# Performance work log

Measured on AMD Instinct MI355X. Metric: run time of the kernel, lower is better.

Reference implementation:

```python
import jax, jax.numpy as jnp
import numpy as np
from jax import lax

NUM_ANCHORS = 3
NUM_CLASSES = 80
SCORE_THRESH = 0.3
NMS_THRESH = 0.45
TOPK = 128  # max kept candidates per class per image (fixed-shape NMS)
REDUCTIONS = (8, 16, 32)
_ANCHORS = np.array([[12, 16], [19, 36], [40, 28], [36, 75], [76, 55], [72, 146],
                     [142, 110], [192, 243], [459, 401]], dtype=np.float32).reshape(3, 3, 2)


def _decode(pred, anchors):
    # pred: [b, A*(5+C), h, w]; anchors: [A,2] already divided by reduction
    b, c, h, w = pred.shape
    p = pred.reshape(b, NUM_ANCHORS, 5 + NUM_CLASSES, h * w).transpose(0, 1, 3, 2)  # [b,A,hw,5+C]
    gx = (jnp.arange(h * w) % w).astype(p.dtype)   # grid x offset per flattened cell
    gy = (jnp.arange(h * w) // w).astype(p.dtype)  # grid y offset
    cx = (jax.nn.sigmoid(p[..., 0]) + gx) / w
    cy = (jax.nn.sigmoid(p[..., 1]) + gy) / h
    bw = jnp.exp(p[..., 2]) * (anchors[:, 0] / w)[None, :, None]
    bh = jnp.exp(p[..., 3]) * (anchors[:, 1] / h)[None, :, None]
    x1 = cx - 0.5 * bw
    y1 = cy - 0.5 * bh
    boxes = jnp.stack([x1, y1, x1 + bw, y1 + bh], axis=-1)  # [b,A,hw,4] xyxy, normalized
    scores = jax.nn.sigmoid(p[..., 4])[..., None] * jax.nn.sigmoid(p[..., 5:])  # [b,A,hw,C]
    return boxes, scores


def _nms_single(boxes, probs):
    # boxes: [N,4]; probs: [N] with below-threshold entries masked to -1.
    # Greedy NMS on top-K candidates sorted by score (same math as the numpy loop).
    vals, idx = lax.top_k(probs, TOPK)
    bx = boxes[idx]                                            # [K,4] sorted by score desc
    area = (bx[:, 2] - bx[:, 0]) * (bx[:, 3] - bx[:, 1])
    tl = jnp.maximum(bx[:, None, :2], bx[None, :, :2])
    br = jnp.minimum(bx[:, None, 2:], bx[None, :, 2:])
    whi = jnp.clip(br - tl, 0.0)
    inter = whi[..., 0] * whi[..., 1]
    iou = inter / (area[:, None] + area[None, :] - inter)      # [K,K]
    ar = jnp.arange(TOPK)

    def step(p, i):
        sup = (iou[i] > NMS_THRESH) & (ar > i) & (p[i] > 0)
        return jnp.where(sup, -1.0, p), None

    p, _ = lax.scan(step, vals, ar)
    keep = p > 0
    return jnp.where(keep[:, None], bx, 0.0), jnp.where(keep, p, 0.0)


def reference(preds0, preds1, preds2):
    boxes_list, score_list = [], []
    for pred, red, anc in zip((preds0, preds1, preds2), REDUCTIONS, _ANCHORS):
        bx, sc = _decode(pred, jnp.asarray(anc) / red)
        boxes_list.append(bx)
        score_list.append(sc)
    boxes = jnp.concatenate(boxes_list, axis=2)
    scores = jnp.concatenate(score_list, axis=2)
    b = boxes.shape[0]
    boxes = boxes.reshape(b, -1, 4)              # [b, N, 4],  N = A * sum(hw)
    scores = scores.reshape(b, -1, NUM_CLASSES)  # [b, N, C]
    probs = jnp.where(scores > SCORE_THRESH, scores, -1.0)
    per_class = jax.vmap(_nms_single, in_axes=(None, 1))        # map over classes
    out_boxes, out_scores = jax.vmap(per_class)(boxes, probs)   # [b,C,K,4], [b,C,K]
    cls_id = jnp.broadcast_to(
        jnp.arange(NUM_CLASSES, dtype=out_boxes.dtype)[None, :, None], out_scores.shape)
    # [b, C, K, 6] = (x1, y1, x2, y2, score, class_id); zeroed rows = no detection
    return jnp.concatenate([out_boxes, out_scores[..., None], cls_id[..., None]], axis=-1)


def setup_inputs():
    key = jax.random.key(0)
    k0, k1, k2 = jax.random.split(key, 3)
    C = NUM_ANCHORS * (5 + NUM_CLASSES)
    return {
        "preds0": jax.random.normal(k0, (16, C, 76, 76), jnp.float32),
        "preds1": jax.random.normal(k1, (16, C, 38, 38), jnp.float32),
        "preds2": jax.random.normal(k2, (16, C, 19, 19), jnp.float32),
    }
```

## Files before the change

kernel.cpp:

```cpp
#include <hip/hip_runtime.h>
#include <math.h>
#include <stdint.h>

#define BATCH 16
#define NCLS 80
#define SUMHW 7581
#define NN 22743
#define ASTRIDE 7584
#define PADNN (3 * ASTRIDE)
#define TOPK 128
#define CAP 1024
#define WCAP 320
#define GMAX (4 * WCAP)
#define PRUNECAP 512
#define KEYBASE 0x3E800000u
#define KB2     0x3F180000u
#define SBITS   0x3F19999Au

typedef float f32x4 __attribute__((ext_vector_type(4)));

__device__ __forceinline__ float sigf(float x) {
    float e = (float)exp(-(double)x);
    return 1.0f / (1.0f + e);
}
__device__ __forceinline__ float expf_cr(float x) {
    return (float)exp((double)x);
}

struct DecParams { float aw[9]; float ah[9]; };

__global__ __launch_bounds__(256) void decode_kernel(
        const float* __restrict__ p0, const float* __restrict__ p1,
        const float* __restrict__ p2,
        float* __restrict__ so_arr, float* __restrict__ xthr_arr) {
    int blk = blockIdx.x;
    int b = blk / 27;
    int rem = blk % 27;
    int a = rem / 9;
    int seg = rem % 9;
    int s, segi;
    if (seg < 6)      { s = 0; segi = seg; }
    else if (seg < 8) { s = 1; segi = seg - 6; }
    else              { s = 2; segi = 0; }
    const int HW_[3]  = {5776, 1444, 361};
    const int OFF_[3] = {0, 5776, 7220};
    const float* __restrict__ pr = (s == 0) ? p0 : (s == 1) ? p1 : p2;
    int HW = HW_[s], OFF = OFF_[s];
    int t = threadIdx.x;

    auto mkthr = [](float so) {
        float thr = __int_as_float(0x7F800000);
        if (so > 0.59999f) {
            double arg = (double)so / 0.59999 - 1.0;
            thr = __double2float_rd(-log(arg));
        }
        return thr;
    };

    if (s != 2) {
        int cell0 = segi * 1024 + t * 4;
        if (cell0 >= HW) return;
        const float4* ob4 =
            (const float4*)(pr + ((size_t)b * 255 + (size_t)a * 85 + 4) * (size_t)HW);
        float4 ov = ob4[cell0 >> 2];
        float4 sov, thv;
        sov.x = sigf(ov.x); thv.x = mkthr(sov.x);
        sov.y = sigf(ov.y); thv.y = mkthr(sov.y);
        sov.z = sigf(ov.z); thv.z = mkthr(sov.z);
        sov.w = sigf(ov.w); thv.w = mkthr(sov.w);
        size_t pidx = (size_t)b * PADNN + a * ASTRIDE + OFF + cell0;
        *(float4*)(so_arr + pidx)   = sov;
        *(float4*)(xthr_arr + pidx) = thv;
    } else {
        const float* ob = pr + ((size_t)b * 255 + (size_t)a * 85 + 4) * 361;
        for (int i = t; i < 361; i += 256) {
            float so = sigf(ob[i]);
            size_t pidx = (size_t)b * PADNN + a * ASTRIDE + 7220 + i;
            so_arr[pidx] = so;
            xthr_arr[pidx] = mkthr(so);
        }
    }
}

__global__ __launch_bounds__(256) void select_nms_kernel(
        const float* __restrict__ p0, const float* __restrict__ p1,
        const float* __restrict__ p2,
        const float* __restrict__ so_arr,
        const float* __restrict__ xthr_arr,
        DecParams dp,
        float* __restrict__ out) {
    __shared__ __attribute__((aligned(16))) unsigned long long wn64[4 * WCAP];
    unsigned long long* skeyF = wn64;
    __shared__ unsigned int kbuf[GMAX];
    __shared__ unsigned long long skeyM[PRUNECAP];
    __shared__ unsigned long long sorted[TOPK];
    __shared__ unsigned long long mskp[2 * TOPK];
    __shared__ float4 bxs4[TOPK];
    __shared__ float pvs[TOPK];
    __shared__ unsigned int hist[512];
    __shared__ unsigned int sums[256];
    __shared__ unsigned int wvc[4];
    __shared__ unsigned long long aliveLDS[2];
    __shared__ unsigned int sh_bin, sh_above, gcount;

    int t = threadIdx.x;
    int w = t >> 6, lane = t & 63;
    int bid = blockIdx.x;
    int b = bid / NCLS;
    int c = bid % NCLS;

    if (t < 4) wvc[t] = 0;
    for (int i = t; i < 512; i += 256) hist[i] = 0;
    __syncthreads();

    auto cmpPushB = [&](f32x4 A0, f32x4 A1, f32x4 A2,
                        f32x4 Q0, f32x4 Q1, f32x4 Q2, int cellb) {
        unsigned m = 0;
        m |= (A0.x > Q0.x) ? 0x001u : 0u;  m |= (A0.y > Q0.y) ? 0x002u : 0u;
        m |= (A0.z > Q0.z) ? 0x004u : 0u;  m |= (A0.w > Q0.w) ? 0x008u : 0u;
        m |= (A1.x > Q1.x) ? 0x010u : 0u;  m |= (A1.y > Q1.y) ? 0x020u : 0u;
        m |= (A1.z > Q1.z) ? 0x040u : 0u;  m |= (A1.w > Q1.w) ? 0x080u : 0u;
        m |= (A2.x > Q2.x) ? 0x100u : 0u;  m |= (A2.y > Q2.y) ? 0x200u : 0u;
        m |= (A2.z > Q2.z) ? 0x400u : 0u;  m |= (A2.w > Q2.w) ? 0x800u : 0u;
        if (m) {
            unsigned pos = atomicAdd(&wvc[w], (unsigned)__popc(m));
            unsigned long long* wl = wn64 + w * WCAP;
#define PKW(bit, val, nn) \
            if (m & (bit)) { if (pos < WCAP) wl[pos] = \
                (((unsigned long long)__float_as_uint(val)) << 32) | (unsigned)(nn); \
                pos++; }
            PKW(0x001u, A0.x, cellb + 0)
            PKW(0x002u, A0.y, cellb + 1)
            PKW(0x004u, A0.z, cellb + 2)
            PKW(0x008u, A0.w, cellb + 3)
            PKW(0x010u, A1.x, SUMHW + cellb + 0)
            PKW(0x020u, A1.y, SUMHW + cellb + 1)
            PKW(0x040u, A1.z, SUMHW + cellb + 2)
            PKW(0x080u, A1.w, SUMHW + cellb + 3)
            PKW(0x100u, A2.x, 2 * SUMHW + cellb + 0)
            PKW(0x200u, A2.y, 2 * SUMHW + cellb + 1)
            PKW(0x400u, A2.z, 2 * SUMHW + cellb + 2)
            PKW(0x800u, A2.w, 2 * SUMHW + cellb + 3)
#undef PKW
        }
    };

    auto scanBlock = [&](const float* __restrict__ pr, int HW, int OFF) {
        const int nq = HW >> 2;
        unsigned long long bx0 = (unsigned long long)(uintptr_t)
            (pr + ((size_t)b * 255 + 0 * 85 + 5 + (size_t)c) * (size_t)HW);
        unsigned long long bx1 = (unsigned long long)(uintptr_t)
            (pr + ((size_t)b * 255 + 1 * 85 + 5 + (size_t)c) * (size_t)HW);
        unsigned long long bx2 = (unsigned long long)(uintptr_t)
            (pr + ((size_t)b * 255 + 2 * 85 + 5 + (size_t)c) * (size_t)HW);
        unsigned long long bq0 = (unsigned long long)(uintptr_t)
            (xthr_arr + (size_t)b * PADNN + 0 * ASTRIDE + OFF);
        unsigned long long bq1 = (unsigned long long)(uintptr_t)
            (xthr_arr + (size_t)b * PADNN + 1 * ASTRIDE + OFF);
        unsigned long long bq2 = (unsigned long long)(uintptr_t)
            (xthr_arr + (size_t)b * PADNN + 2 * ASTRIDE + OFF);
        int i = t;
        for (; i + 256 < nq; i += 512) {
            unsigned vo1 = (unsigned)i << 4;
            unsigned vo2 = (unsigned)(i + 256) << 4;
            f32x4 x0, x1, x2, x3, x4, x5, q0, q1, q2, q3, q4, q5;
            asm volatile(
                "global_load_dwordx4 %0, %12, %14\n\t"
                "global_load_dwordx4 %1, %12, %15\n\t"
                "global_load_dwordx4 %2, %12, %16\n\t"
                "global_load_dwordx4 %3, %13, %14\n\t"
                "global_load_dwordx4 %4, %13, %15\n\t"
                "global_load_dwordx4 %5, %13, %16\n\t"
                "global_load_dwordx4 %6, %12, %17\n\t"
                "global_load_dwordx4 %7, %12, %18\n\t"
                "global_load_dwordx4 %8, %12, %19\n\t"
                "global_load_dwordx4 %9, %13, %17\n\t"
                "global_load_dwordx4 %10, %13, %18\n\t"
                "global_load_dwordx4 %11, %13, %19\n\t"
                "s_waitcnt vmcnt(0)"
                : "=&v"(x0), "=&v"(x1), "=&v"(x2), "=&v"(x3), "=&v"(x4), "=&v"(x5),
                  "=&v"(q0), "=&v"(q1), "=&v"(q2), "=&v"(q3), "=&v"(q4), "=&v"(q5)
                : "v"(vo1), "v"(vo2), "s"(bx0), "s"(bx1), "s"(bx2),
                  "s"(bq0), "s"(bq1), "s"(bq2));
            cmpPushB(x0, x1, x2, q0, q1, q2, OFF + 4 * i);
            cmpPushB(x3, x4, x5, q3, q4, q5, OFF + 4 * (i + 256));
        }
        if (i < nq) {
            unsigned voff = (unsigned)i << 4;
            f32x4 x0, x1, x2, q0, q1, q2;
            asm volatile(
                "global_load_dwordx4 %0, %6, %7\n\t"
                "global_load_dwordx4 %1, %6, %8\n\t"
                "global_load_dwordx4 %2, %6, %9\n\t"
                "global_load_dwordx4 %3, %6, %10\n\t"
                "global_load_dwordx4 %4, %6, %11\n\t"
                "global_load_dwordx4 %5, %6, %12\n\t"
                "s_waitcnt vmcnt(0)"
                : "=&v"(x0), "=&v"(x1), "=&v"(x2),
                  "=&v"(q0), "=&v"(q1), "=&v"(q2)
                : "v"(voff), "s"(bx0), "s"(bx1), "s"(bx2),
                  "s"(bq0), "s"(bq1), "s"(bq2));
            cmpPushB(x0, x1, x2, q0, q1, q2, OFF + 4 * i);
        }
    };
    scanBlock(p0, 5776, 0);
    scanBlock(p1, 1444, 5776);
#pragma unroll
    for (int a = 0; a < 3; ++a) {
        const float* __restrict__ cp =
            p2 + ((size_t)b * 255 + (size_t)a * 85 + 5 + (size_t)c) * 361;
        const float* __restrict__ xt = xthr_arr + (size_t)b * PADNN + a * ASTRIDE + 7220;
        int n0 = a * SUMHW + 7220;
        for (int i = t; i < 361; i += 256) {
            float xv = cp[i];
            if (xv > xt[i]) {
                unsigned pos = atomicAdd(&wvc[w], 1u);
                if (pos < WCAP) wn64[w * WCAP + pos] =
                    (((unsigned long long)__float_as_uint(xv)) << 32) | (unsigned)(n0 + i);
            }
        }
    }
    __syncthreads();

    unsigned cw0 = wvc[0], cw1 = wvc[1], cw2 = wvc[2], cw3 = wvc[3];
    bool ovf = (cw0 > WCAP) || (cw1 > WCAP) || (cw2 > WCAP) || (cw3 > WCAP);
    unsigned G = cw0 + cw1 + cw2 + cw3;
    bool fb = ovf || (G < TOPK);

    auto rankSelect = [&](const unsigned long long* sk, unsigned Gc) {
        if (t < TOPK) sorted[t] = 0ULL;
        __syncthreads();
        unsigned i0 = t, i1 = t + 256, i2 = t + 512, i3 = t + 768;
        bool v0 = i0 < Gc, v1 = i1 < Gc, v2 = i2 < Gc, v3 = i3 < Gc;
        unsigned long long o0 = v0 ? sk[i0] : 0ULL;
        unsigned long long o1 = v1 ? sk[i1] : 0ULL;
        unsigned long long o2 = v2 ? sk[i2] : 0ULL;
        unsigned long long o3 = v3 ? sk[i3] : 0ULL;
        unsigned r0 = 0, r1 = 0, r2 = 0, r3 = 0;
        for (unsigned j = 0; j < Gc; ++j) {
            unsigned long long kj = sk[j];
            r0 += (kj > o0); r1 += (kj > o1); r2 += (kj > o2); r3 += (kj > o3);
        }
        if (v0 && r0 < TOPK) sorted[r0] = o0;
        if (v1 && r1 < TOPK) sorted[r1] = o1;
        if (v2 && r2 < TOPK) sorted[r2] = o2;
        if (v3 && r3 < TOPK) sorted[r3] = o3;
        __syncthreads();
    };

    if (!fb) {
        unsigned woff = 0;
        if (w > 0) woff += cw0;
        if (w > 1) woff += cw1;
        if (w > 2) woff += cw2;
        unsigned mycnt = (w == 0) ? cw0 : (w == 1) ? cw1 : (w == 2) ? cw2 : cw3;
        for (unsigned i = lane; i < mycnt; i += 64) {
            unsigned long long e = wn64[w * WCAP + i];
            float x = __uint_as_float((unsigned)(e >> 32));
            unsigned n = (unsigned)(e & 0xFFFFFFFFu);
            unsigned a = n / SUMHW;
            unsigned r = n - a * SUMHW;
            float so = so_arr[(size_t)b * PADNN + a * ASTRIDE + r];
            float st = 1.0f / (1.0f + __expf(-x));
            unsigned key = __float_as_uint(st * so);
            kbuf[woff + i] = key;
            unsigned bin = (key - KB2) >> 14;
            if (bin > 511u) bin = 511u;
            atomicAdd(&hist[bin], 1u);
        }
        if (t == 0) gcount = 0;
        __syncthreads();

        unsigned m0 = hist[2 * t], m1 = hist[2 * t + 1];
        sums[t] = m0 + m1;
        __syncthreads();
        for (int d = 1; d < 256; d <<= 1) {
            unsigned v = sums[t];
            if (t + d < 256) v += sums[t + d];
            __syncthreads();
            sums[t] = v;
            __syncthreads();
        }
        unsigned si = sums[t], se = si - (m0 + m1);
        if (se < TOPK && TOPK <= si) {
            if (TOPK <= se + m1) { sh_bin = 2 * t + 1; sh_above = se; }
            else                 { sh_bin = 2 * t;     sh_above = se + m1; }
        }
        __syncthreads();
        unsigned B1 = sh_bin, above1 = sh_above;
        unsigned cntB = hist[B1];
        unsigned binlo = KB2 + (B1 << 14);
        if (above1 + cntB > PRUNECAP - 64) {
            fb = true;
        } else {
            unsigned gth = binlo - 256;
            unsigned b1e = cw0, b2e = cw0 + cw1, b3e = b2e + cw2;
            for (unsigned i = t; i < G; i += 256) {
                if (kbuf[i] >= gth) {
                    unsigned pos = atomicAdd(&gcount, 1u);
                    if (pos < PRUNECAP) {
                        unsigned w2, off2;
                        if (i < b1e)      { w2 = 0; off2 = i; }
                        else if (i < b2e) { w2 = 1; off2 = i - b1e; }
                        else if (i < b3e) { w2 = 2; off2 = i - b2e; }
                        else              { w2 = 3; off2 = i - b3e; }
                        unsigned long long e = wn64[w2 * WCAP + off2];
                        float x = __uint_as_float((unsigned)(e >> 32));
                        unsigned n = (unsigned)(e & 0xFFFFFFFFu);
                        unsigned a = n / SUMHW;
                        unsigned r = n - a * SUMHW;
                        float so = so_arr[(size_t)b * PADNN + a * ASTRIDE + r];
                        float ex = so * sigf(x);
                        skeyM[pos] = (ex > 0.3f)
                            ? (((unsigned long long)__float_as_uint(ex) << 32) |
                               (unsigned)(~n))
                            : (unsigned long long)(unsigned)(~n);
                    }
                }
            }
            __syncthreads();
            if (gcount > PRUNECAP) fb = true;
            if (!fb) {
                unsigned Gc = gcount;
                rankSelect(skeyM, Gc);
                bool ok = (Gc >= TOPK) && ((unsigned)(sorted[TOPK - 1] >> 32) >= SBITS);
                if (!ok) fb = true;
            }
        }
    }

    if (fb) {
        auto scanScalar = [&](auto&& body) {
#pragma unroll
            for (int s = 0; s < 3; ++s) {
                const float* __restrict__ pr = (s == 0) ? p0 : (s == 1) ? p1 : p2;
                const int HW  = (s == 0) ? 5776 : (s == 1) ? 1444 : 361;
                const int OFF = (s == 0) ? 0 : (s == 1) ? 5776 : 7220;
#pragma unroll
                for (int a = 0; a < 3; ++a) {
                    const float* __restrict__ cp =
                        pr + ((size_t)b * 255 + (size_t)a * 85 + 5 + (size_t)c) * (size_t)HW;
                    const float* __restrict__ sop =
                        so_arr + (size_t)b * PADNN + a * ASTRIDE + OFF;
                    int n0 = a * SUMHW + OFF;
                    for (int i = t; i < HW; i += 256) {
                        float so = sop[i];
                        if (so <= 0.2999f) continue;
                        float x = cp[i];
                        float st = 1.0f / (1.0f + __expf(-x));
                        float sca = st * so;
                        if (sca > 0.2999f) body(sca, x, so, n0 + i);
                    }
                }
            }
        };
        __syncthreads();
        for (int i = t; i < 512; i += 256) hist[i] = 0;
        if (t == 0) gcount = 0;
        __syncthreads();
        scanScalar([&](float sca, float, float, int) {
            unsigned bin = (__float_as_uint(sca) - KEYBASE) >> 15;
            if (bin > 511u) bin = 511u;
            atomicAdd(&hist[bin], 1u);
        });
        __syncthreads();
        unsigned m0 = hist[2 * t], m1 = hist[2 * t + 1];
        sums[t] = m0 + m1;
        __syncthreads();
        for (int d = 1; d < 256; d <<= 1) {
            unsigned v = sums[t];
            if (t + d < 256) v += sums[t + d];
            __syncthreads();
            sums[t] = v;
            __syncthreads();
        }
        unsigned total = sums[0];
        bool gatherAll = (total < TOPK);
        unsigned gth = 0;
        if (!gatherAll) {
            unsigned si = sums[t], se = si - (m0 + m1);
            if (se < TOPK && TOPK <= si) {
                if (TOPK <= se + m1) { sh_bin = 2 * t + 1; sh_above = se; }
                else                 { sh_bin = 2 * t;     sh_above = se + m1; }
            }
            __syncthreads();
            unsigned B1 = sh_bin, above1 = sh_above;
            unsigned cntB = hist[B1];
            unsigned binlo = KEYBASE + (B1 << 15);
            __syncthreads();
            if (above1 + cntB <= 768) {
                gth = binlo - 256;
            } else {
                if (t < 256) hist[t] = 0;
                __syncthreads();
                scanScalar([&](float sca, float, float, int) {
                    unsigned key = __float_as_uint(sca);
                    if (((key - KEYBASE) >> 15) == B1) {
                        unsigned sub = (key - binlo) >> 7;
                        if (sub > 255u) sub = 255u;
                        atomicAdd(&hist[sub], 1u);
                    }
                });
                __syncthreads();
                unsigned R2 = TOPK - above1;
                unsigned sl = hist[t];
                sums[t] = sl;
                __syncthreads();
                for (int d = 1; d < 256; d <<= 1) {
                    unsigned v = sums[t];
                    if (t + d < 256) v += sums[t + d];
                    __syncthreads();
                    sums[t] = v;
                    __syncthreads();
                }
                unsigned si2 = sums[t], se2 = si2 - sl;
                if (se2 < R2 && R2 <= si2) sh_bin = (unsigned)t;
                __syncthreads();
                gth = binlo + (sh_bin << 7) - 256;
            }
        }
        __syncthreads();
        scanScalar([&](float sca, float x, float so, int n) {
            unsigned key = __float_as_uint(sca);
            if (gatherAll || key >= gth) {
                unsigned pos = atomicAdd(&gcount, 1u);
                if (pos < CAP) {
                    float ex = so * sigf(x);
                    skeyF[pos] = (ex > 0.3f)
                        ? (((unsigned long long)__float_as_uint(ex) << 32) |
                           (unsigned)(~(unsigned)n))
                        : (unsigned long long)(unsigned)(~(unsigned)n);
                }
            }
        });
        __syncthreads();
        unsigned Gc = gcount < CAP ? gcount : CAP;
        rankSelect(skeyF, Gc);
    }

    if (t < TOPK) {
        unsigned long long e = sorted[t];
        bool vld = (e != 0ULL);
        float sc = __uint_as_float((unsigned)(e >> 32));
        unsigned n = ~(unsigned)(e & 0xFFFFFFFFu);
        float4 bb = make_float4(0.f, 0.f, 0.f, 0.f);
        if (vld) {
            unsigned a = n / SUMHW;
            unsigned r = n - a * SUMHW;
            int s, S, HW, off; const float* pr;
            if (r < 5776u)      { s = 0; S = 76; HW = 5776; off = 0;    pr = p0; }
            else if (r < 7220u) { s = 1; S = 38; HW = 1444; off = 5776; pr = p1; }
            else                { s = 2; S = 19; HW = 361;  off = 7220; pr = p2; }
            int cell = (int)r - off;
            const float* pb = pr + ((size_t)b * 255 + (size_t)a * 85) * (size_t)HW + cell;
            float tx = pb[0];
            float ty = pb[(size_t)HW];
            float tw = pb[(size_t)2 * HW];
            float th = pb[(size_t)3 * HW];
            float Sf = (float)S;
            float gx = (float)(cell % S);
            float gy = (float)(cell / S);
            float cx = (sigf(tx) + gx) / Sf;
            float cy = (sigf(ty) + gy) / Sf;
            float aw = dp.aw[s * 3 + a], ah = dp.ah[s * 3 + a];
            float bw = expf_cr(tw) * aw;
            float bh = expf_cr(th) * ah;
            float x1 = cx - 0.5f * bw;
            float y1 = cy - 0.5f * bh;
            bb = make_float4(x1, y1, x1 + bw, y1 + bh);
        }
        bxs4[t] = bb;
        pvs[t] = vld ? sc : -1.0f;
    }
    __syncthreads();

    {
        int i = t >> 1, h = t & 1;
        float4 bi = bxs4[i];
        float ai = (bi.z - bi.x) * (bi.w - bi.y);
        unsigned long long m = 0;
        int jb = h << 6;
        for (int k = 0; k < 64; ++k) {
            int j = jb + k;
            float4 bj = bxs4[j];
            float aj = (bj.z - bj.x) * (bj.w - bj.y);
            float xx1 = fmaxf(bi.x, bj.x), yy1 = fmaxf(bi.y, bj.y);
            float xx2 = fminf(bi.z, bj.z), yy2 = fminf(bi.w, bj.w);
            float ww = fmaxf(xx2 - xx1, 0.0f), hh = fmaxf(yy2 - yy1, 0.0f);
            float inter = ww * hh;
            float iou = inter / (ai + aj - inter);
            if (j > i && iou > 0.45f) m |= (1ull << k);
        }
        mskp[(i << 1) | h] = m;
    }
    __syncthreads();
    if (t < 64) {
        unsigned long long A0 = __ballot(pvs[t] > 0.0f);
        unsigned long long A1 = __ballot(pvs[t + 64] > 0.0f);
        for (int i = 0; i < 64; ++i) {
            if ((A0 >> i) & 1) { A0 &= ~mskp[i << 1]; A1 &= ~mskp[(i << 1) | 1]; }
        }
        for (int i = 0; i < 64; ++i) {
            if ((A1 >> i) & 1) { A1 &= ~mskp[((64 + i) << 1) | 1]; }
        }
        if (t == 0) { aliveLDS[0] = A0; aliveLDS[1] = A1; }
    }
    __syncthreads();

    unsigned long long A0 = aliveLDS[0], A1 = aliveLDS[1];
    float* o = out + (size_t)bid * TOPK * 6;
    for (int i = t; i < TOPK; i += 256) {
        bool alive = (i < 64) ? ((A0 >> i) & 1) : ((A1 >> (i - 64)) & 1);
        float p = pvs[i];
        bool kept = alive && (p > 0.0f);
        float4 bb = bxs4[i];
        o[i * 6 + 0] = kept ? bb.x : 0.0f;
        o[i * 6 + 1] = kept ? bb.y : 0.0f;
        o[i * 6 + 2] = kept ? bb.z : 0.0f;
        o[i * 6 + 3] = kept ? bb.w : 0.0f;
        o[i * 6 + 4] = kept ? p : 0.0f;
        o[i * 6 + 5] = (float)c;
    }
}

extern "C" void kernel_launch(void* const* d_in, const int* in_sizes, int n_in,
                              void* d_out, int out_size, void* d_ws, size_t ws_size,
                              hipStream_t stream) {
    const float* p0 = (const float*)d_in[0];
    const float* p1 = (const float*)d_in[1];
    const float* p2 = (const float*)d_in[2];
    float* out = (float*)d_out;

    char* ws = (char*)d_ws;
    float* so_arr = (float*)ws;
    float* xthr   = (float*)(ws + 1456128ull);

    static const float ANC[3][3][2] = {
        {{12, 16}, {19, 36}, {40, 28}},
        {{36, 75}, {76, 55}, {72, 146}},
        {{142, 110}, {192, 243}, {459, 401}},
    };
    static const int RED[3] = {8, 16, 32};
    static const int SS[3]  = {76, 38, 19};

    DecParams dp;
    for (int s = 0; s < 3; ++s)
        for (int a = 0; a < 3; ++a) {
            float Sf = (float)SS[s];
            dp.aw[s * 3 + a] = (ANC[s][a][0] / (float)RED[s]) / Sf;
            dp.ah[s * 3 + a] = (ANC[s][a][1] / (float)RED[s]) / Sf;
        }

    decode_kernel<<<BATCH * 27, 256, 0, stream>>>(p0, p1, p2, so_arr, xthr);
    select_nms_kernel<<<BATCH * NCLS, 256, 0, stream>>>(p0, p1, p2, so_arr, xthr, dp, out);
}
```

Measured before the change: 67.43 us.

## Use wave-level scans for candidate push and histogram prefix sums

```diff
diff --git a/kernel.cpp b/kernel.cpp
--- a/kernel.cpp
+++ b/kernel.cpp
@@ -98,7 +98,7 @@
     __shared__ float4 bxs4[TOPK];
     __shared__ float pvs[TOPK];
     __shared__ unsigned int hist[512];
-    __shared__ unsigned int sums[256];
+    __shared__ unsigned int wtot[4];
     __shared__ unsigned int wvc[4];
     __shared__ unsigned long long aliveLDS[2];
     __shared__ unsigned int sh_bin, sh_above, gcount;
@@ -113,17 +113,20 @@
     for (int i = t; i < 512; i += 256) hist[i] = 0;
     __syncthreads();
 
-    auto cmpPushB = [&](f32x4 A0, f32x4 A1, f32x4 A2,
-                        f32x4 Q0, f32x4 Q1, f32x4 Q2, int cellb) {
-        unsigned m = 0;
-        m |= (A0.x > Q0.x) ? 0x001u : 0u;  m |= (A0.y > Q0.y) ? 0x002u : 0u;
-        m |= (A0.z > Q0.z) ? 0x004u : 0u;  m |= (A0.w > Q0.w) ? 0x008u : 0u;
-        m |= (A1.x > Q1.x) ? 0x010u : 0u;  m |= (A1.y > Q1.y) ? 0x020u : 0u;
-        m |= (A1.z > Q1.z) ? 0x040u : 0u;  m |= (A1.w > Q1.w) ? 0x080u : 0u;
-        m |= (A2.x > Q2.x) ? 0x100u : 0u;  m |= (A2.y > Q2.y) ? 0x200u : 0u;
-        m |= (A2.z > Q2.z) ? 0x400u : 0u;  m |= (A2.w > Q2.w) ? 0x800u : 0u;
-        if (m) {
-            unsigned pos = atomicAdd(&wvc[w], (unsigned)__popc(m));
+    auto wavePush = [&](unsigned m, f32x4 A0, f32x4 A1, f32x4 A2, int cellb) {
+        unsigned cnt = (unsigned)__popc(m);
+        unsigned inc = cnt;
+#pragma unroll
+        for (int d = 1; d < 64; d <<= 1) {
+            unsigned o = (unsigned)__shfl_up((int)inc, d);
+            if (lane >= d) inc += o;
+        }
+        unsigned wt = (unsigned)__shfl((int)inc, 63);
+        if (wt) {
+            unsigned base = 0;
+            if (lane == 63) base = atomicAdd(&wvc[w], wt);
+            base = (unsigned)__shfl((int)base, 63);
+            unsigned pos = base + inc - cnt;
             unsigned long long* wl = wn64 + w * WCAP;
 #define PKW(bit, val, nn) \
             if (m & (bit)) { if (pos < WCAP) wl[pos] = \
@@ -144,6 +147,17 @@
 #undef PKW
         }
     };
+    auto cmpMask = [&](f32x4 A0, f32x4 A1, f32x4 A2,
+                       f32x4 Q0, f32x4 Q1, f32x4 Q2) -> unsigned {
+        unsigned m = 0;
+        m |= (A0.x > Q0.x) ? 0x001u : 0u;  m |= (A0.y > Q0.y) ? 0x002u : 0u;
+        m |= (A0.z > Q0.z) ? 0x004u : 0u;  m |= (A0.w > Q0.w) ? 0x008u : 0u;
+        m |= (A1.x > Q1.x) ? 0x010u : 0u;  m |= (A1.y > Q1.y) ? 0x020u : 0u;
+        m |= (A1.z > Q1.z) ? 0x040u : 0u;  m |= (A1.w > Q1.w) ? 0x080u : 0u;
+        m |= (A2.x > Q2.x) ? 0x100u : 0u;  m |= (A2.y > Q2.y) ? 0x200u : 0u;
+        m |= (A2.z > Q2.z) ? 0x400u : 0u;  m |= (A2.w > Q2.w) ? 0x800u : 0u;
+        return m;
+    };
 
     auto scanBlock = [&](const float* __restrict__ pr, int HW, int OFF) {
         const int nq = HW >> 2;
@@ -159,10 +173,13 @@
             (xthr_arr + (size_t)b * PADNN + 1 * ASTRIDE + OFF);
         unsigned long long bq2 = (unsigned long long)(uintptr_t)
             (xthr_arr + (size_t)b * PADNN + 2 * ASTRIDE + OFF);
-        int i = t;
-        for (; i + 256 < nq; i += 512) {
-            unsigned vo1 = (unsigned)i << 4;
-            unsigned vo2 = (unsigned)(i + 256) << 4;
+        const int nIter = (nq + 511) >> 9;
+        for (int k2 = 0; k2 < nIter; ++k2) {
+            int i1 = t + (k2 << 9);
+            int i2 = i1 + 256;
+            bool a1 = i1 < nq, a2 = i2 < nq;
+            unsigned vo1 = (unsigned)(a1 ? i1 : (nq - 1)) << 4;
+            unsigned vo2 = (unsigned)(a2 ? i2 : (nq - 1)) << 4;
             f32x4 x0, x1, x2, x3, x4, x5, q0, q1, q2, q3, q4, q5;
             asm volatile(
                 "global_load_dwordx4 %0, %12, %14\n\t"
@@ -182,25 +199,10 @@
                   "=&v"(q0), "=&v"(q1), "=&v"(q2), "=&v"(q3), "=&v"(q4), "=&v"(q5)
                 : "v"(vo1), "v"(vo2), "s"(bx0), "s"(bx1), "s"(bx2),
                   "s"(bq0), "s"(bq1), "s"(bq2));
-            cmpPushB(x0, x1, x2, q0, q1, q2, OFF + 4 * i);
-            cmpPushB(x3, x4, x5, q3, q4, q5, OFF + 4 * (i + 256));
-        }
-        if (i < nq) {
-            unsigned voff = (unsigned)i << 4;
-            f32x4 x0, x1, x2, q0, q1, q2;
-            asm volatile(
-                "global_load_dwordx4 %0, %6, %7\n\t"
-                "global_load_dwordx4 %1, %6, %8\n\t"
-                "global_load_dwordx4 %2, %6, %9\n\t"
-                "global_load_dwordx4 %3, %6, %10\n\t"
-                "global_load_dwordx4 %4, %6, %11\n\t"
-                "global_load_dwordx4 %5, %6, %12\n\t"
-                "s_waitcnt vmcnt(0)"
-                : "=&v"(x0), "=&v"(x1), "=&v"(x2),
-                  "=&v"(q0), "=&v"(q1), "=&v"(q2)
-                : "v"(voff), "s"(bx0), "s"(bx1), "s"(bx2),
-                  "s"(bq0), "s"(bq1), "s"(bq2));
-            cmpPushB(x0, x1, x2, q0, q1, q2, OFF + 4 * i);
+            unsigned m1 = cmpMask(x0, x1, x2, q0, q1, q2); if (!a1) m1 = 0;
+            unsigned m2 = cmpMask(x3, x4, x5, q3, q4, q5); if (!a2) m2 = 0;
+            wavePush(m1, x0, x1, x2, OFF + 4 * i1);
+            wavePush(m2, x3, x4, x5, OFF + 4 * i2);
         }
     };
     scanBlock(p0, 5776, 0);
@@ -227,24 +229,60 @@
     unsigned G = cw0 + cw1 + cw2 + cw3;
     bool fb = ovf || (G < TOPK);
 
-    auto rankSelect = [&](const unsigned long long* sk, unsigned Gc) {
+    auto suffixScan = [&](unsigned mt, unsigned& total) -> unsigned {
+        __syncthreads();
+        unsigned sfx = mt;
+#pragma unroll
+        for (int d = 1; d < 64; d <<= 1) {
+            unsigned o = (unsigned)__shfl_down((int)sfx, d);
+            if (lane + d < 64) sfx += o;
+        }
+        if (lane == 0) wtot[w] = sfx;
+        __syncthreads();
+        unsigned cross = 0;
+#pragma unroll
+        for (int ww = 0; ww < 4; ++ww) if (ww > w) cross += wtot[ww];
+        total = wtot[0] + wtot[1] + wtot[2] + wtot[3];
+        return sfx + cross;
+    };
+
+    auto rankSelect2 = [&](const unsigned long long* sk, unsigned Gc) {
         if (t < TOPK) sorted[t] = 0ULL;
         __syncthreads();
-        unsigned i0 = t, i1 = t + 256, i2 = t + 512, i3 = t + 768;
-        bool v0 = i0 < Gc, v1 = i1 < Gc, v2 = i2 < Gc, v3 = i3 < Gc;
-        unsigned long long o0 = v0 ? sk[i0] : 0ULL;
-        unsigned long long o1 = v1 ? sk[i1] : 0ULL;
-        unsigned long long o2 = v2 ? sk[i2] : 0ULL;
-        unsigned long long o3 = v3 ? sk[i3] : 0ULL;
-        unsigned r0 = 0, r1 = 0, r2 = 0, r3 = 0;
-        for (unsigned j = 0; j < Gc; ++j) {
-            unsigned long long kj = sk[j];
-            r0 += (kj > o0); r1 += (kj > o1); r2 += (kj > o2); r3 += (kj > o3);
-        }
-        if (v0 && r0 < TOPK) sorted[r0] = o0;
-        if (v1 && r1 < TOPK) sorted[r1] = o1;
-        if (v2 && r2 < TOPK) sorted[r2] = o2;
-        if (v3 && r3 < TOPK) sorted[r3] = o3;
+        if ((unsigned)t < Gc) {
+            unsigned long long o0 = sk[t];
+            bool v1 = (unsigned)(t + 256) < Gc;
+            unsigned long long o1 = v1 ? sk[t + 256] : 0ULL;
+            unsigned r0 = 0, r1 = 0;
+            for (unsigned j = 0; j < Gc; ++j) {
+                unsigned long long kj = sk[j];
+                r0 += (kj > o0); r1 += (kj > o1);
+            }
+            if (r0 < TOPK) sorted[r0] = o0;
+            if (v1 && r1 < TOPK) sorted[r1] = o1;
+        }
+        __syncthreads();
+    };
+    auto rankSelect4 = [&](const unsigned long long* sk, unsigned Gc) {
+        if (t < TOPK) sorted[t] = 0ULL;
+        __syncthreads();
+        if ((unsigned)t < Gc) {
+            unsigned i1 = t + 256, i2 = t + 512, i3 = t + 768;
+            bool v1 = i1 < Gc, v2 = i2 < Gc, v3 = i3 < Gc;
+            unsigned long long o0 = sk[t];
+            unsigned long long o1 = v1 ? sk[i1] : 0ULL;
+            unsigned long long o2 = v2 ? sk[i2] : 0ULL;
+            unsigned long long o3 = v3 ? sk[i3] : 0ULL;
+            unsigned r0 = 0, r1 = 0, r2 = 0, r3 = 0;
+            for (unsigned j = 0; j < Gc; ++j) {
+                unsigned long long kj = sk[j];
+                r0 += (kj > o0); r1 += (kj > o1); r2 += (kj > o2); r3 += (kj > o3);
+            }
+            if (r0 < TOPK) sorted[r0] = o0;
+            if (v1 && r1 < TOPK) sorted[r1] = o1;
+            if (v2 && r2 < TOPK) sorted[r2] = o2;
+            if (v3 && r3 < TOPK) sorted[r3] = o3;
+        }
         __syncthreads();
     };
 
@@ -272,16 +310,9 @@
         __syncthreads();
 
         unsigned m0 = hist[2 * t], m1 = hist[2 * t + 1];
-        sums[t] = m0 + m1;
-        __syncthreads();
-        for (int d = 1; d < 256; d <<= 1) {
-            unsigned v = sums[t];
-            if (t + d < 256) v += sums[t + d];
-            __syncthreads();
-            sums[t] = v;
-            __syncthreads();
-        }
-        unsigned si = sums[t], se = si - (m0 + m1);
+        unsigned total;
+        unsigned si = suffixScan(m0 + m1, total);
+        unsigned se = si - (m0 + m1);
         if (se < TOPK && TOPK <= si) {
             if (TOPK <= se + m1) { sh_bin = 2 * t + 1; sh_above = se; }
             else                 { sh_bin = 2 * t;     sh_above = se + m1; }
@@ -322,7 +353,7 @@
             if (gcount > PRUNECAP) fb = true;
             if (!fb) {
                 unsigned Gc = gcount;
-                rankSelect(skeyM, Gc);
+                rankSelect2(skeyM, Gc);
                 bool ok = (Gc >= TOPK) && ((unsigned)(sorted[TOPK - 1] >> 32) >= SBITS);
                 if (!ok) fb = true;
             }
@@ -365,20 +396,12 @@
         });
         __syncthreads();
         unsigned m0 = hist[2 * t], m1 = hist[2 * t + 1];
-        sums[t] = m0 + m1;
-        __syncthreads();
-        for (int d = 1; d < 256; d <<= 1) {
-            unsigned v = sums[t];
-            if (t + d < 256) v += sums[t + d];
-            __syncthreads();
-            sums[t] = v;
-            __syncthreads();
-        }
-        unsigned total = sums[0];
+        unsigned total;
+        unsigned si = suffixScan(m0 + m1, total);
         bool gatherAll = (total < TOPK);
         unsigned gth = 0;
         if (!gatherAll) {
-            unsigned si = sums[t], se = si - (m0 + m1);
+            unsigned se = si - (m0 + m1);
             if (se < TOPK && TOPK <= si) {
                 if (TOPK <= se + m1) { sh_bin = 2 * t + 1; sh_above = se; }
                 else                 { sh_bin = 2 * t;     sh_above = se + m1; }
@@ -404,16 +427,9 @@
                 __syncthreads();
                 unsigned R2 = TOPK - above1;
                 unsigned sl = hist[t];
-                sums[t] = sl;
-                __syncthreads();
-                for (int d = 1; d < 256; d <<= 1) {
-                    unsigned v = sums[t];
-                    if (t + d < 256) v += sums[t + d];
-                    __syncthreads();
-                    sums[t] = v;
-                    __syncthreads();
-                }
-                unsigned si2 = sums[t], se2 = si2 - sl;
+                unsigned tot2;
+                unsigned si2 = suffixScan(sl, tot2);
+                unsigned se2 = si2 - sl;
                 if (se2 < R2 && R2 <= si2) sh_bin = (unsigned)t;
                 __syncthreads();
                 gth = binlo + (sh_bin << 7) - 256;
@@ -435,7 +451,7 @@
         });
         __syncthreads();
         unsigned Gc = gcount < CAP ? gcount : CAP;
-        rankSelect(skeyF, Gc);
+        rankSelect4(skeyF, Gc);
     }
 
     if (t < TOPK) {
@@ -476,20 +492,23 @@
 
     {
         int i = t >> 1, h = t & 1;
-        float4 bi = bxs4[i];
-        float ai = (bi.z - bi.x) * (bi.w - bi.y);
         unsigned long long m = 0;
-        int jb = h << 6;
-        for (int k = 0; k < 64; ++k) {
-            int j = jb + k;
-            float4 bj = bxs4[j];
-            float aj = (bj.z - bj.x) * (bj.w - bj.y);
-            float xx1 = fmaxf(bi.x, bj.x), yy1 = fmaxf(bi.y, bj.y);
-            float xx2 = fminf(bi.z, bj.z), yy2 = fminf(bi.w, bj.w);
-            float ww = fmaxf(xx2 - xx1, 0.0f), hh = fmaxf(yy2 - yy1, 0.0f);
-            float inter = ww * hh;
-            float iou = inter / (ai + aj - inter);
-            if (j > i && iou > 0.45f) m |= (1ull << k);
+        if (!(h == 0 && i >= 64)) {
+            float4 bi = bxs4[i];
+            float ai = (bi.z - bi.x) * (bi.w - bi.y);
+            int jb = h << 6;
+            int kstart = (h == 0) ? (i + 1) : ((i >= 64) ? (i - 63) : 0);
+            for (int k = kstart; k < 64; ++k) {
+                int j = jb + k;
+                float4 bj = bxs4[j];
+                float aj = (bj.z - bj.x) * (bj.w - bj.y);
+                float xx1 = fmaxf(bi.x, bj.x), yy1 = fmaxf(bi.y, bj.y);
+                float xx2 = fminf(bi.z, bj.z), yy2 = fminf(bi.w, bj.w);
+                float ww = fmaxf(xx2 - xx1, 0.0f), hh = fmaxf(yy2 - yy1, 0.0f);
+                float inter = ww * hh;
+                float iou = inter / (ai + aj - inter);
+                if (j > i && iou > 0.45f) m |= (1ull << k);
+            }
         }
         mskp[(i << 1) | h] = m;
     }
```

Measured after the change: 68.15 us. Within noise of the previous version (+1.1%).
